# Performance work log

Hardware: AMD Instinct MI355X
Metric: run time of the kernel (lower is better)

Reference implementation:

```python
import jax, jax.numpy as jnp
import numpy as np

NX, NY = 512, 512
DX, DY = 1e-4, 1e-4
VS = 1550.0
DT = 2.5e-8


def setup_inputs() -> dict:
    key = jax.random.key(0)
    k1, k2 = jax.random.split(key)
    sensor_data = jax.random.normal(k1, (4, 2, 128, 2048), dtype=jnp.float32)
    sensor_xy = jax.random.randint(k2, (128, 2), 0, 512, dtype=jnp.int32)
    return {"sensor_data": sensor_data, "sensor_xy": sensor_xy}


def _delay_indices(sensor_xy):
    # pixel grids, 1-indexed as in the torch code (arange(1,513))
    ix = jnp.arange(1, NX + 1, dtype=jnp.float32)[None, :, None]  # (1,Nx,1)
    iy = jnp.arange(1, NY + 1, dtype=jnp.float32)[None, None, :]  # (1,1,Ny)
    x = sensor_xy[:, 0].astype(jnp.float32)[:, None, None]        # (S,1,1)
    y = sensor_xy[:, 1].astype(jnp.float32)[:, None, None]
    dis = jnp.sqrt(((x - ix + 1.0) * DX) ** 2 + ((y - iy + 1.0) * DY) ** 2)  # (S,Nx,Ny)
    # .to(torch.long) truncates; values are non-negative so int cast matches
    return (dis / VS / DT).astype(jnp.int32).reshape(sensor_xy.shape[0], -1)  # (S, Nx*Ny)


def reference(sensor_data, sensor_xy):
    B = sensor_data.shape[0]
    S = sensor_xy.shape[0]
    t = _delay_indices(sensor_xy)                           # (S, P) int32
    data = jnp.transpose(sensor_data, (2, 0, 1, 3))         # (S, B, 2, T)

    def step(img, xs):
        t_s, d_s = xs                                       # (P,), (B,2,T)
        return img + d_s[:, :, t_s], None                   # gather + accumulate

    img0 = jnp.zeros((B, 2, NX * NY), dtype=sensor_data.dtype)
    img, _ = jax.lax.scan(step, img0, (t, data))
    return img.reshape(B, 2, NX, NY)
```

## Files before the change

kernel.cpp:

```cpp
#include <hip/hip_runtime.h>
#include <math.h>


#define NXY 512
#define S_CNT 128
#define T_CNT 2048
#define CH 8
#define CH_STRIDE (S_CNT * T_CNT)
#define NPIX (NXY * NXY)
#define NTILE 1024
#define TAB_BYTES (NPIX * 2)
#define D2B_BYTES (CH_STRIDE * 16)
#define META_BYTES (NTILE * S_CNT * 16)
#define CHUNK 8
#define NCHUNK (S_CNT / CHUNK)
#define WIN 64
#define PATW 24
#define PAT_SENS_B (16 * PATW * 2)

typedef float f32x2 __attribute__((ext_vector_type(2)));

#if __has_builtin(__builtin_amdgcn_sad_u32)
__device__ __forceinline__ unsigned int sadu(unsigned int a, unsigned int b, unsigned int c) {
    return __builtin_amdgcn_sad_u32(a, b, c);
}
#else
__device__ __forceinline__ unsigned int sadu(unsigned int a, unsigned int b, unsigned int c) {
    return (a > b ? a - b : b - a) + c;
}
#endif

__device__ __forceinline__ unsigned short delay_entry(int adx, int ady) {
    const double DX32 = (double)1e-4f;
    const double R1 = (double)(float)(1.0 / 1550.0);
    const double R2 = (double)(float)(1.0 / (double)2.5e-8f);
    float dxf = (float)((double)adx * DX32);
    float dyf = (float)((double)ady * DX32);
    float a2 = (float)((double)dxf * (double)dxf);
    float b2 = (float)((double)dyf * (double)dyf);
    float sum = (float)((double)a2 + (double)b2);
    float dis = (float)sqrt((double)sum);
    float q1 = (float)((double)dis * R1);
    float q2 = (float)((double)q1 * R2);
    return (unsigned short)(int)q2;
}

__device__ __forceinline__ unsigned int bf16_rne(float f) {
    unsigned int x = __float_as_uint(f);
    return (x + 0x7fffu + ((x >> 16) & 1u)) >> 16;
}

__global__ __launch_bounds__(256) void prep(const float* __restrict__ data,
                                            const int* __restrict__ sxy,
                                            unsigned short* __restrict__ tab,
                                            uint4* __restrict__ d2b,
                                            uint4* __restrict__ meta) {
    int idx = blockIdx.x * 256 + threadIdx.x;
    tab[idx] = (unsigned short)((unsigned int)delay_entry(idx >> 9, idx & 511) << 4);

    unsigned int w[4];
#pragma unroll
    for (int j = 0; j < 4; ++j) {
        unsigned int lo = bf16_rne(data[(2 * j) * CH_STRIDE + idx]);
        unsigned int hi = bf16_rne(data[(2 * j + 1) * CH_STRIDE + idx]);
        w[j] = lo | (hi << 16);
    }
    d2b[idx] = make_uint4(w[0], w[1], w[2], w[3]);

    if (idx < NTILE * S_CNT) {
        int tile = idx >> 7;
        int s = idx & 127;
        int x0 = (tile >> 5) << 4;
        int y0 = (tile & 31) << 4;
        int sxv = sxy[2 * s];
        int syv = sxy[2 * s + 1];
        int axm = sxv < x0 ? x0 - sxv : (sxv > x0 + 15 ? sxv - x0 - 15 : 0);
        int aym = syv < y0 ? y0 - syv : (syv > y0 + 15 ? syv - y0 - 15 : 0);
        int ay0 = aym & ~7;
        int tmin = (int)delay_entry(axm, aym);
        meta[idx] = make_uint4((unsigned int)sxv, (unsigned int)(2 * syv),
                               (unsigned int)(axm | (ay0 << 16)),
                               (unsigned int)(tmin << 4));
    }
}

__device__ __forceinline__ float bflo(unsigned int u) { return __uint_as_float(u << 16); }
__device__ __forceinline__ float bfhi(unsigned int u) { return __uint_as_float(u & 0xffff0000u); }

__device__ __forceinline__ unsigned int swz16(unsigned int d) {
    return d ^ (((d >> 7) & 3u) << 4);
}
__device__ __forceinline__ unsigned int subswz_x2(unsigned int a, unsigned int tm4) {
    unsigned int lo = swz16((a - tm4) & 0xffffu);
    unsigned int hi = swz16(((a >> 16) - tm4) & 0xffffu);
    return lo | (hi << 16);
}

__global__ __launch_bounds__(256) void das_smeta(const uint4* __restrict__ d2b,
                                                 const uint4* __restrict__ meta,
                                                 float* __restrict__ out) {
    __shared__ uint2 mstage[S_CNT];
    __shared__ uint4 winb[2][CHUNK * WIN];
    __shared__ uint4 patb[2][CHUNK * 16 * 3];

    int tid = threadIdx.x;
    const uint4* mblk = meta + ((size_t)blockIdx.x << 7);

    if (tid < S_CNT) {
        uint4 m = mblk[tid];
        mstage[tid] = make_uint2(m.z, m.w);
    }
    __syncthreads();

    int y0 = (blockIdx.x & 31) << 4;
    int x0 = (blockIdx.x >> 5) << 4;
    int iy = y0 | (((tid >> 6) & 1) << 3) | (tid & 7);
    int ix = x0 | ((tid >> 7) << 3) | ((tid >> 3) & 7);
    unsigned int uix = (unsigned int)ix;
    unsigned int uiy2 = (unsigned int)(2 * iy);

    f32x2 acc2[4];
#pragma unroll
    for (int k = 0; k < 4; ++k) acc2[k] = (f32x2){0.0f, 0.0f};

    uint4 rw0, rw1;
    uint4 rp0, rp1;
    unsigned int wslot, pslot0, pslot1, ptm0, ptm1;
    const int lsw = tid >> 5, e0 = tid & 31;
    const unsigned int swn = (((unsigned int)e0 >> 3) & 3u) << 4;
    const bool p1act = tid < 128;

#define ISSUE(cc)                                                                     \
    {                                                                                 \
        int s0n = (cc) * CHUNK;                                                       \
        uint2 stw = mstage[s0n + lsw];                                                \
        const uint4* wsrc = d2b + ((size_t)(s0n + lsw) << 11) + (stw.y >> 4) + e0;    \
        rw0 = wsrc[0];                                                                \
        rw1 = wsrc[32];                                                               \
        wslot = ((unsigned int)lsw << 10) | (((unsigned int)e0 << 4) ^ swn);          \
        {                                                                             \
            unsigned int pidx = (unsigned int)tid;                                    \
            unsigned int r3 = pidx / 3u, cc2 = pidx - r3 * 3u;                        \
            unsigned int row = r3 & 15u, ls = r3 >> 4;                                \
            uint2 stp = mstage[s0n + ls];                                             \
            rp0 = *(const uint4*)((const char*)tab_g +                                \
                ((((stp.x & 0xffffu) + row) << 10) + ((stp.x >> 16) << 1) + (cc2 << 4))); \
            pslot0 = ls * 768u + row * 48u + cc2 * 16u;                               \
            ptm0 = stp.y;                                                             \
        }                                                                             \
        if (p1act) {                                                                  \
            unsigned int pidx = (unsigned int)tid + 256u;                             \
            unsigned int r3 = pidx / 3u, cc2 = pidx - r3 * 3u;                        \
            unsigned int row = r3 & 15u, ls = r3 >> 4;                                \
            uint2 stp = mstage[s0n + ls];                                             \
            rp1 = *(const uint4*)((const char*)tab_g +                                \
                ((((stp.x & 0xffffu) + row) << 10) + ((stp.x >> 16) << 1) + (cc2 << 4))); \
            pslot1 = ls * 768u + row * 48u + cc2 * 16u;                               \
            ptm1 = stp.y;                                                             \
        }                                                                             \
    }

#define WRITEBUF(cc)                                                                  \
    {                                                                                 \
        char* wb = (char*)winb[(cc) & 1];                                             \
        char* pb = (char*)patb[(cc) & 1];                                             \
        *(uint4*)(wb + wslot) = rw0;                                                  \
        *(uint4*)(wb + wslot + 512u) = rw1;                                           \
        uint4 v = rp0;                                                                \
        v.x = subswz_x2(v.x, ptm0);                                                   \
        v.y = subswz_x2(v.y, ptm0);                                                   \
        v.z = subswz_x2(v.z, ptm0);                                                   \
        v.w = subswz_x2(v.w, ptm0);                                                   \
        *(uint4*)(pb + pslot0) = v;                                                   \
        if (p1act) {                                                                  \
            uint4 u = rp1;                                                            \
            u.x = subswz_x2(u.x, ptm1);                                               \
            u.y = subswz_x2(u.y, ptm1);                                               \
            u.z = subswz_x2(u.z, ptm1);                                               \
            u.w = subswz_x2(u.w, ptm1);                                               \
            *(uint4*)(pb + pslot1) = u;                                               \
        }                                                                             \
    }

    const char* tab_g = (const char*)d2b - TAB_BYTES;

    ISSUE(0);
    WRITEBUF(0);
    __syncthreads();

    for (int c = 0; c < NCHUNK; ++c) {
        if (c + 1 < NCHUNK) ISSUE(c + 1);

        {
            const char* patc = (const char*)patb[c & 1];
            const char* winc = (const char*)winb[c & 1];
            int s0 = c * CHUNK;
            unsigned int t16[CHUNK];
#pragma unroll
            for (int j = 0; j < CHUNK; ++j) {
                uint4 m = mblk[s0 + j];
                unsigned int Cc = 0u - ((m.z & 0xffffu) * 48u + (m.z >> 16) * 2u);
                unsigned int b1 = sadu(m.x, uix, 0u);
                unsigned int b2 = sadu(m.y, uiy2, 0u);
                unsigned int byte = b1 * 48u + b2 + Cc;
                t16[j] = (unsigned int)*(const unsigned short*)(
                    patc + (unsigned int)(j * PAT_SENS_B) + byte);
            }
#pragma unroll
            for (int j = 0; j < CHUNK; ++j) {
                uint4 w = *(const uint4*)(winc + (unsigned int)(j << 10) + t16[j]);
                f32x2 p0 = {bflo(w.x), bfhi(w.x)};
                f32x2 p1 = {bflo(w.y), bfhi(w.y)};
                f32x2 p2 = {bflo(w.z), bfhi(w.z)};
                f32x2 p3 = {bflo(w.w), bfhi(w.w)};
                acc2[0] += p0;
                acc2[1] += p1;
                acc2[2] += p2;
                acc2[3] += p3;
            }
        }

        if (c + 1 < NCHUNK) WRITEBUF(c + 1);
        __syncthreads();
    }
#undef ISSUE
#undef WRITEBUF

    int pix = (ix << 9) | iy;
#pragma unroll
    for (int k = 0; k < 4; ++k) {
        out[(2 * k) * NPIX + pix] = acc2[k].x;
        out[(2 * k + 1) * NPIX + pix] = acc2[k].y;
    }
}

__global__ __launch_bounds__(256) void build_table(unsigned short* __restrict__ tab) {
    int idx = blockIdx.x * 256 + threadIdx.x;
    tab[idx] = delay_entry(idx >> 9, idx & 511);
}

__global__ __launch_bounds__(256) void das_main(const float* __restrict__ data,
                                                const unsigned short* __restrict__ tab,
                                                const int* __restrict__ sxy,
                                                float* __restrict__ out) {
    __shared__ int sx[S_CNT];
    __shared__ int sy[S_CNT];
    int tid = threadIdx.x;
    if (tid < S_CNT) {
        sx[tid] = sxy[2 * tid];
        sy[tid] = sxy[2 * tid + 1];
    }
    __syncthreads();
    int iy = ((blockIdx.x & 31) << 4) | (tid & 15);
    int ix = ((blockIdx.x >> 5) << 4) | (tid >> 4);
    float acc[CH];
#pragma unroll
    for (int k = 0; k < CH; ++k) acc[k] = 0.0f;
#pragma unroll 4
    for (int s = 0; s < S_CNT; ++s) {
        int dxi = sx[s] - ix;
        int dyi = sy[s] - iy;
        int adx = dxi < 0 ? -dxi : dxi;
        int ady = dyi < 0 ? -dyi : dyi;
        int t = (int)tab[(adx << 9) | ady];
        const float* p = data + (s << 11) + t;
#pragma unroll
        for (int k = 0; k < CH; ++k) acc[k] += p[(size_t)k * CH_STRIDE];
    }
    int pix = (ix << 9) | iy;
#pragma unroll
    for (int k = 0; k < CH; ++k) out[k * NPIX + pix] = acc[k];
}

extern "C" void kernel_launch(void* const* d_in, const int* in_sizes, int n_in,
                              void* d_out, int out_size, void* d_ws, size_t ws_size,
                              hipStream_t stream) {
    const float* data = (const float*)d_in[0];
    const int* sxy = (const int*)d_in[1];
    float* out = (float*)d_out;
    unsigned short* tab = (unsigned short*)d_ws;

    size_t need = (size_t)TAB_BYTES + (size_t)D2B_BYTES + (size_t)META_BYTES;
    if (ws_size >= need) {
        uint4* d2b = (uint4*)((char*)d_ws + TAB_BYTES);
        uint4* meta = (uint4*)((char*)d_ws + TAB_BYTES + D2B_BYTES);
        prep<<<NPIX / 256, 256, 0, stream>>>(data, sxy, tab, d2b, meta);
        das_smeta<<<NTILE, 256, 0, stream>>>(d2b, meta, out);
    } else {
        build_table<<<NPIX / 256, 256, 0, stream>>>(tab);
        das_main<<<1024, 256, 0, stream>>>(data, tab, sxy, out);
    }
}
```

Baseline: 100.8 us.

## Split sensor loop across two blocks per tile and combine partial sums

Each pixel tile is now handled by two blocks, one per half of the sensors, and each block writes its partial sums to a workspace buffer. A separate combine kernel adds the two partials into the output. Per-block staging shrinks to 4 sensors per pass, and each thread issues one window load and at most one pattern load per pass. The aim is more blocks in flight and higher occupancy to hide gather latency, at the cost of 16 MB of extra partial writes and reads plus one more kernel launch.

```diff
diff --git a/kernel.cpp b/kernel.cpp
--- a/kernel.cpp
+++ b/kernel.cpp
@@ -12,8 +12,10 @@
 #define TAB_BYTES (NPIX * 2)
 #define D2B_BYTES (CH_STRIDE * 16)
 #define META_BYTES (NTILE * S_CNT * 16)
-#define CHUNK 8
-#define NCHUNK (S_CNT / CHUNK)
+#define PART_BYTES (2 * CH * NPIX * 4)
+#define HCNT 64
+#define CHUNK 4
+#define NPASS (HCNT / CHUNK)
 #define WIN 64
 #define PATW 24
 #define PAT_SENS_B (16 * PATW * 2)
@@ -96,24 +98,27 @@
     return lo | (hi << 16);
 }
 
-__global__ __launch_bounds__(256) void das_smeta(const uint4* __restrict__ d2b,
+__global__ __launch_bounds__(256) void das_ghalf(const uint4* __restrict__ d2b,
                                                  const uint4* __restrict__ meta,
-                                                 float* __restrict__ out) {
-    __shared__ uint2 mstage[S_CNT];
+                                                 float* __restrict__ part) {
+    __shared__ uint2 mstage[HCNT];
     __shared__ uint4 winb[2][CHUNK * WIN];
     __shared__ uint4 patb[2][CHUNK * 16 * 3];
 
     int tid = threadIdx.x;
-    const uint4* mblk = meta + ((size_t)blockIdx.x << 7);
-
-    if (tid < S_CNT) {
+    int tile = blockIdx.x >> 1;
+    int h = blockIdx.x & 1;
+    const uint4* mblk = meta + ((size_t)tile << 7) + ((size_t)h << 6);
+    const uint4* d2bh = d2b + ((size_t)(h * HCNT) << 11);
+
+    if (tid < HCNT) {
         uint4 m = mblk[tid];
         mstage[tid] = make_uint2(m.z, m.w);
     }
     __syncthreads();
 
-    int y0 = (blockIdx.x & 31) << 4;
-    int x0 = (blockIdx.x >> 5) << 4;
+    int y0 = (tile & 31) << 4;
+    int x0 = (tile >> 5) << 4;
     int iy = y0 | (((tid >> 6) & 1) << 3) | (tid & 7);
     int ix = x0 | ((tid >> 7) << 3) | ((tid >> 3) & 7);
     unsigned int uix = (unsigned int)ix;
@@ -123,40 +128,29 @@
 #pragma unroll
     for (int k = 0; k < 4; ++k) acc2[k] = (f32x2){0.0f, 0.0f};
 
-    uint4 rw0, rw1;
-    uint4 rp0, rp1;
-    unsigned int wslot, pslot0, pslot1, ptm0, ptm1;
-    const int lsw = tid >> 5, e0 = tid & 31;
+    uint4 rw0, rp0;
+    unsigned int wslot, pslot0, ptm0;
+    const int lsw = tid >> 6, e0 = tid & 63;
     const unsigned int swn = (((unsigned int)e0 >> 3) & 3u) << 4;
-    const bool p1act = tid < 128;
+    const bool pact = tid < 192;
+
+    const char* tab_g = (const char*)d2b - TAB_BYTES;
 
 #define ISSUE(cc)                                                                     \
     {                                                                                 \
         int s0n = (cc) * CHUNK;                                                       \
         uint2 stw = mstage[s0n + lsw];                                                \
-        const uint4* wsrc = d2b + ((size_t)(s0n + lsw) << 11) + (stw.y >> 4) + e0;    \
-        rw0 = wsrc[0];                                                                \
-        rw1 = wsrc[32];                                                               \
+        rw0 = d2bh[((size_t)(s0n + lsw) << 11) + (stw.y >> 4) + e0];                  \
         wslot = ((unsigned int)lsw << 10) | (((unsigned int)e0 << 4) ^ swn);          \
-        {                                                                             \
+        if (pact) {                                                                   \
             unsigned int pidx = (unsigned int)tid;                                    \
             unsigned int r3 = pidx / 3u, cc2 = pidx - r3 * 3u;                        \
             unsigned int row = r3 & 15u, ls = r3 >> 4;                                \
             uint2 stp = mstage[s0n + ls];                                             \
-            rp0 = *(const uint4*)((const char*)tab_g +                                \
+            rp0 = *(const uint4*)(tab_g +                                             \
                 ((((stp.x & 0xffffu) + row) << 10) + ((stp.x >> 16) << 1) + (cc2 << 4))); \
             pslot0 = ls * 768u + row * 48u + cc2 * 16u;                               \
             ptm0 = stp.y;                                                             \
-        }                                                                             \
-        if (p1act) {                                                                  \
-            unsigned int pidx = (unsigned int)tid + 256u;                             \
-            unsigned int r3 = pidx / 3u, cc2 = pidx - r3 * 3u;                        \
-            unsigned int row = r3 & 15u, ls = r3 >> 4;                                \
-            uint2 stp = mstage[s0n + ls];                                             \
-            rp1 = *(const uint4*)((const char*)tab_g +                                \
-                ((((stp.x & 0xffffu) + row) << 10) + ((stp.x >> 16) << 1) + (cc2 << 4))); \
-            pslot1 = ls * 768u + row * 48u + cc2 * 16u;                               \
-            ptm1 = stp.y;                                                             \
         }                                                                             \
     }
 
@@ -165,31 +159,22 @@
         char* wb = (char*)winb[(cc) & 1];                                             \
         char* pb = (char*)patb[(cc) & 1];                                             \
         *(uint4*)(wb + wslot) = rw0;                                                  \
-        *(uint4*)(wb + wslot + 512u) = rw1;                                           \
-        uint4 v = rp0;                                                                \
-        v.x = subswz_x2(v.x, ptm0);                                                   \
-        v.y = subswz_x2(v.y, ptm0);                                                   \
-        v.z = subswz_x2(v.z, ptm0);                                                   \
-        v.w = subswz_x2(v.w, ptm0);                                                   \
-        *(uint4*)(pb + pslot0) = v;                                                   \
-        if (p1act) {                                                                  \
-            uint4 u = rp1;                                                            \
-            u.x = subswz_x2(u.x, ptm1);                                               \
-            u.y = subswz_x2(u.y, ptm1);                                               \
-            u.z = subswz_x2(u.z, ptm1);                                               \
-            u.w = subswz_x2(u.w, ptm1);                                               \
-            *(uint4*)(pb + pslot1) = u;                                               \
+        if (pact) {                                                                   \
+            uint4 v = rp0;                                                            \
+            v.x = subswz_x2(v.x, ptm0);                                               \
+            v.y = subswz_x2(v.y, ptm0);                                               \
+            v.z = subswz_x2(v.z, ptm0);                                               \
+            v.w = subswz_x2(v.w, ptm0);                                               \
+            *(uint4*)(pb + pslot0) = v;                                               \
         }                                                                             \
     }
-
-    const char* tab_g = (const char*)d2b - TAB_BYTES;
 
     ISSUE(0);
     WRITEBUF(0);
     __syncthreads();
 
-    for (int c = 0; c < NCHUNK; ++c) {
-        if (c + 1 < NCHUNK) ISSUE(c + 1);
+    for (int c = 0; c < NPASS; ++c) {
+        if (c + 1 < NPASS) ISSUE(c + 1);
 
         {
             const char* patc = (const char*)patb[c & 1];
@@ -220,18 +205,28 @@
             }
         }
 
-        if (c + 1 < NCHUNK) WRITEBUF(c + 1);
+        if (c + 1 < NPASS) WRITEBUF(c + 1);
         __syncthreads();
     }
 #undef ISSUE
 #undef WRITEBUF
 
+    float* outp = part + (size_t)h * (CH * NPIX);
     int pix = (ix << 9) | iy;
 #pragma unroll
     for (int k = 0; k < 4; ++k) {
-        out[(2 * k) * NPIX + pix] = acc2[k].x;
-        out[(2 * k + 1) * NPIX + pix] = acc2[k].y;
-    }
+        outp[(2 * k) * NPIX + pix] = acc2[k].x;
+        outp[(2 * k + 1) * NPIX + pix] = acc2[k].y;
+    }
+}
+
+__global__ __launch_bounds__(256) void combine(const float4* __restrict__ p0,
+                                               const float4* __restrict__ p1,
+                                               float4* __restrict__ out) {
+    int i = blockIdx.x * 256 + threadIdx.x;
+    float4 a = p0[i];
+    float4 b = p1[i];
+    out[i] = make_float4(a.x + b.x, a.y + b.y, a.z + b.z, a.w + b.w);
 }
 
 __global__ __launch_bounds__(256) void build_table(unsigned short* __restrict__ tab) {
@@ -280,12 +275,16 @@
     float* out = (float*)d_out;
     unsigned short* tab = (unsigned short*)d_ws;
 
-    size_t need = (size_t)TAB_BYTES + (size_t)D2B_BYTES + (size_t)META_BYTES;
+    size_t need = (size_t)TAB_BYTES + (size_t)D2B_BYTES + (size_t)META_BYTES +
+                  (size_t)PART_BYTES;
     if (ws_size >= need) {
         uint4* d2b = (uint4*)((char*)d_ws + TAB_BYTES);
         uint4* meta = (uint4*)((char*)d_ws + TAB_BYTES + D2B_BYTES);
+        float* part = (float*)((char*)d_ws + TAB_BYTES + D2B_BYTES + META_BYTES);
         prep<<<NPIX / 256, 256, 0, stream>>>(data, sxy, tab, d2b, meta);
-        das_smeta<<<NTILE, 256, 0, stream>>>(d2b, meta, out);
+        das_ghalf<<<2 * NTILE, 256, 0, stream>>>(d2b, meta, part);
+        combine<<<CH * NPIX / 1024, 256, 0, stream>>>(
+            (const float4*)part, (const float4*)(part + CH * NPIX), (float4*)out);
     } else {
         build_table<<<NPIX / 256, 256, 0, stream>>>(tab);
         das_main<<<1024, 256, 0, stream>>>(data, tab, sxy, out);
```

After: 99.59 us. No clear change (-1.2%).
